# Kernel optimization log

Measured on AMD Instinct MI355X. Metric: run time of the kernel, lower is better.

Reference implementation:

```python
import jax, jax.numpy as jnp
import numpy as np

B, S, E, H, MAXLEN = 2, 2048, 1024, 16, 2048


def _level_indices(seq_len: int, base: int = 2) -> np.ndarray:
    """Vectorized version of get_level_index_weak over the full (target, source) grid.
    indices[t, s] = min(level, 2) for s < t, else 0. Runs in O(log S) passes."""
    tt = np.broadcast_to(np.arange(seq_len)[:, None], (seq_len, seq_len)).astype(np.int64).copy()
    ss = np.broadcast_to(np.arange(seq_len)[None, :], (seq_len, seq_len)).astype(np.int64).copy()
    res = np.zeros((seq_len, seq_len), np.int64)
    done = ~(ss < tt)  # only source < target positions get a level; rest stay 0
    while not done.all():
        l = np.floor(np.log2(np.maximum(tt, 1).astype(np.float64))).astype(np.int64)
        v = (np.int64(1) << l)
        hit = (~done) & (ss < v)
        res[hit] = l[hit] + 1
        done |= hit
        step = ~done
        tt[step] -= v[step]
        ss[step] -= v[step]
    return np.minimum(res, 2).astype(np.int32)


def setup_inputs() -> dict:
    key = jax.random.key(0)
    ks = jax.random.split(key, 10)
    sc = 0.02
    return {
        "x": jax.random.normal(ks[0], (B, S, E), dtype=jnp.float32),
        "attention_mask": jax.random.randint(ks[1], (B, S), 0, 2, dtype=jnp.int32),
        "level_indices": jnp.asarray(_level_indices(S, 2)),
        "Wq": jax.random.normal(ks[2], (E, E), dtype=jnp.float32) * sc,
        "bq": jnp.zeros((E,), jnp.float32),
        "Wk": jax.random.normal(ks[3], (E, E), dtype=jnp.float32) * sc,
        "bk": jnp.zeros((E,), jnp.float32),
        "Wv": jax.random.normal(ks[4], (E, E), dtype=jnp.float32) * sc,
        "bv": jnp.zeros((E,), jnp.float32),
        "hier": jax.random.normal(ks[5], (MAXLEN, H, 3), dtype=jnp.float32),
        "Wo": jax.random.normal(ks[6], (E, E), dtype=jnp.float32) * sc,
        "bo": jnp.zeros((E,), jnp.float32),
    }


def reference(x, attention_mask, level_indices, Wq, bq, Wk, bk, Wv, bv, hier, Wo, bo):
    b, s, e = x.shape
    h = hier.shape[1]
    dh = e // h
    # q/k are computed by the original module but never used; kept for fidelity (zero grads).
    q = x @ Wq.T + bq
    k = x @ Wk.T + bk
    v = (x @ Wv.T + bv).reshape(b, s, h, dh).transpose(0, 2, 1, 3)  # [B,H,S,Dh]
    lev = level_indices[:s, :s]  # [S,S] int, values in {0,1,2}
    # Faithful torch.gather semantics: weights[b,h,i,j] = hier[b, h, lev[i,j]]
    w3 = hier[:b]                      # [B,H,3]
    weights = w3[:, :, lev]            # [B,H,S,S]
    decay = jnp.power(jnp.float32(0.5), lev.astype(x.dtype))  # [S,S]
    weights = weights * decay
    weights = weights / (jnp.sum(weights, axis=-1, keepdims=True) + 1e-8)
    weights = jnp.where(attention_mask[:, None, None, :] == 0, jnp.float32(0.0), weights)
    out = jnp.einsum('bhij,bhjd->bhid', weights, v)  # [B,H,S,Dh]
    out = out.transpose(0, 2, 1, 3).reshape(b, s, e)
    return out @ Wo.T + bo
```

## Files before the change

### kernel.cpp

```cpp
#include <hip/hip_runtime.h>
#include <cstdint>
#include <cstddef>

constexpr int Sn = 2048;
constexpr int En = 1024;
constexpr int Bn = 2;
constexpr int Hn = 16;
constexpr int NCH = 32;
constexpr int CHUNK = 64;
constexpr int Mtot = Bn * Sn;
constexpr int GCH = Mtot / CHUNK;

typedef __bf16 bf16x8 __attribute__((ext_vector_type(8)));
typedef float  f32x4  __attribute__((ext_vector_type(4)));

__device__ __forceinline__ unsigned short f2bf(float f) {
    union { float f; uint32_t u; } v; v.f = f;
    const uint32_t u = v.u;
    return (unsigned short)((u + 0x7fffu + ((u >> 16) & 1u)) >> 16);
}
__device__ __forceinline__ float bf2f_lo(uint32_t u) {
    union { uint32_t u; float f; } v; v.u = u << 16; return v.f;
}
__device__ __forceinline__ float bf2f_hi(uint32_t u) {
    union { uint32_t u; float f; } v; v.u = u & 0xffff0000u; return v.f;
}

constexpr int XN = Bn * Sn * En;
constexpr int WN = En * En;

__global__ __launch_bounds__(256)
void cast3(const float* __restrict__ x, const float* __restrict__ Wv,
           const float* __restrict__ Wo, unsigned short* __restrict__ xb,
           unsigned short* __restrict__ Wvb, unsigned short* __restrict__ Wob)
{
    const int i = (blockIdx.x * 256 + threadIdx.x) * 4;
    const float* src; unsigned short* dst; int off;
    if (i < XN)           { src = x;  dst = xb;  off = i; }
    else if (i < XN + WN) { src = Wv; dst = Wvb; off = i - XN; }
    else                  { src = Wo; dst = Wob; off = i - XN - WN; }
    const float4 v = *(const float4*)(src + off);
    ushort4 o;
    o.x = f2bf(v.x); o.y = f2bf(v.y); o.z = f2bf(v.z); o.w = f2bf(v.w);
    *(ushort4*)(dst + off) = o;
}

#define LOAD6(k0, r0, r1, r2, r3, r4, r5)            \
    r0 = *(const uint4*)(gA0 + (k0));                \
    r1 = *(const uint4*)(gA0 + (k0) + 32);           \
    r2 = *(const uint4*)(gA1 + (k0));                \
    r3 = *(const uint4*)(gA1 + (k0) + 32);           \
    r4 = *(const uint4*)(gB0 + (k0));                \
    r5 = *(const uint4*)(gB0 + (k0) + 32);

#define STORE6(r0, r1, r2, r3, r4, r5)               \
    *lA00 = r0; *lA01 = r1;                          \
    *lA10 = r2; *lA11 = r3;                          \
    *lB00 = r4; *lB01 = r5;

#define COMPUTE()                                                                              \
    {                                                                                          \
        bf16x8 af[4][2], bfr[2][2];                                                            \
        _Pragma("unroll")                                                                      \
        for (int i = 0; i < 4; ++i)                                                            \
            _Pragma("unroll")                                                                  \
            for (int kh = 0; kh < 2; ++kh)                                                     \
                af[i][kh] = *(const bf16x8*)&As[((wr * 4 + i) * 2 + kh) * 512 + lane * 8];      \
        _Pragma("unroll")                                                                      \
        for (int j = 0; j < 2; ++j)                                                            \
            _Pragma("unroll")                                                                  \
            for (int kh = 0; kh < 2; ++kh)                                                     \
                bfr[j][kh] = *(const bf16x8*)&Bs[((wc * 2 + j) * 2 + kh) * 512 + lane * 8];     \
        _Pragma("unroll")                                                                      \
        for (int kh = 0; kh < 2; ++kh)                                                         \
            _Pragma("unroll")                                                                  \
            for (int i = 0; i < 4; ++i)                                                        \
                _Pragma("unroll")                                                              \
                for (int j = 0; j < 2; ++j)                                                    \
                    acc[i][j] = __builtin_amdgcn_mfma_f32_16x16x32_bf16(af[i][kh], bfr[j][kh], \
                                                                        acc[i][j], 0, 0, 0);   \
    }

template<bool APPLY_MASK, bool OUT_BF16, bool FUSE_CSUM>
__global__ __launch_bounds__(256)
void gemm_pipe(const unsigned short* __restrict__ A, const unsigned short* __restrict__ Bw,
               const float* __restrict__ bias, const int* __restrict__ mask,
               void* __restrict__ Cv, float* __restrict__ csum, int M, int N, int K)
{
    __shared__ __align__(16) unsigned short As[128 * 64];
    __shared__ __align__(16) unsigned short Bs[64 * 64];

    const int tid  = threadIdx.x;
    const int lane = tid & 63;
    const int wv   = tid >> 6;
    const int wr   = wv >> 1;
    const int wc   = wv & 1;
    const int bm   = blockIdx.y * 128;
    const int bn   = blockIdx.x * 64;
    const int m16  = lane & 15;
    const int kq   = lane >> 4;

    f32x4 acc[4][2] = {};

    const int rg0 = 2 * wv, rg1 = 2 * wv + 1;
    const unsigned short* gA0 = A  + (size_t)(bm + 16 * rg0 + m16) * K + kq * 8;
    const unsigned short* gA1 = A  + (size_t)(bm + 16 * rg1 + m16) * K + kq * 8;
    const unsigned short* gB0 = Bw + (size_t)(bn + 16 * wv  + m16) * K + kq * 8;
    uint4* lA00 = (uint4*)&As[(rg0 * 2 + 0) * 512 + lane * 8];
    uint4* lA01 = (uint4*)&As[(rg0 * 2 + 1) * 512 + lane * 8];
    uint4* lA10 = (uint4*)&As[(rg1 * 2 + 0) * 512 + lane * 8];
    uint4* lA11 = (uint4*)&As[(rg1 * 2 + 1) * 512 + lane * 8];
    uint4* lB00 = (uint4*)&Bs[(wv  * 2 + 0) * 512 + lane * 8];
    uint4* lB01 = (uint4*)&Bs[(wv  * 2 + 1) * 512 + lane * 8];

    uint4 p0, p1, p2, p3, p4, p5;
    uint4 q0, q1, q2, q3, q4, q5;

    LOAD6(0, p0, p1, p2, p3, p4, p5);
#pragma unroll 1
    for (int it = 0; it < 8; ++it) {
        const int kbase = it * 128;
        __syncthreads();
        STORE6(p0, p1, p2, p3, p4, p5);
        __syncthreads();
        LOAD6(kbase + 64, q0, q1, q2, q3, q4, q5);
        COMPUTE();

        __syncthreads();
        STORE6(q0, q1, q2, q3, q4, q5);
        __syncthreads();
        if (it < 7) { LOAD6(kbase + 128, p0, p1, p2, p3, p4, p5); }
        COMPUTE();
    }

    float colsum[2] = {0.0f, 0.0f};
#pragma unroll
    for (int i = 0; i < 4; ++i) {
        const int r0 = bm + wr * 64 + i * 16 + kq * 4;
#pragma unroll
        for (int j = 0; j < 2; ++j) {
            const int c0 = bn + wc * 32 + j * 16 + m16;
            const float bcol = bias[c0];
#pragma unroll
            for (int r = 0; r < 4; ++r) {
                const int row = r0 + r;
                float val = acc[i][j][r] + bcol;
                if (APPLY_MASK) val = (mask[row] == 0) ? 0.0f : val;
                if (FUSE_CSUM) colsum[j] += val;
                if (OUT_BF16)
                    ((unsigned short*)Cv)[(size_t)row * N + c0] = f2bf(val);
                else
                    ((float*)Cv)[(size_t)row * N + c0] = val;
            }
        }
    }

    if (FUSE_CSUM) {
        const int gc = 2 * blockIdx.y + wr;
#pragma unroll
        for (int j = 0; j < 2; ++j) {
            float s = colsum[j];
            s += __shfl_xor(s, 16, 64);
            s += __shfl_xor(s, 32, 64);
            if (kq == 0)
                csum[(size_t)gc * En + bn + wc * 32 + j * 16 + m16] = s;
        }
    }
}

__global__ __launch_bounds__(256)
void combine(const unsigned short* __restrict__ vm, const float* __restrict__ csum,
             const float* __restrict__ hier, unsigned short* __restrict__ opre)
{
    const int ep = blockIdx.x * 256 + threadIdx.x;
    const int e = ep * 2;
    const int c = blockIdx.y;
    const int b = blockIdx.z;
    const int h = e >> 6;

    const float w0 = hier[((size_t)b * Hn + h) * 3 + 0];
    const float w1 = hier[((size_t)b * Hn + h) * 3 + 1] * 0.5f;
    const float w2 = hier[((size_t)b * Hn + h) * 3 + 2] * 0.25f;

    float run0 = 0.0f, run1 = 0.0f, T0 = 0.0f, T1 = 0.0f;
    const int g0 = b * NCH;
    for (int c2 = 0; c2 < NCH; ++c2) {
        const size_t off = (size_t)(g0 + c2) * En + e;
        const float v0 = csum[off], v1 = csum[off + 1];
        if (c2 < c) { run0 += v0; run1 += v1; }
        T0 += v0; T1 += v1;
    }

    float prev0 = 0.0f, prev1 = 0.0f;
    const size_t base = ((size_t)b * Sn + c * CHUNK) * En + e;

    for (int t = 0; t < CHUNK; ++t) {
        const int i = c * CHUNK + t;
        const uint32_t u = *(const uint32_t*)(vm + base + (size_t)t * En);
        const float cur0 = bf2f_lo(u), cur1 = bf2f_hi(u);
        float num0, num1, Z;
        if (i & 1) {
            num0 = w2 * (run0 - prev0) + w1 * prev0 + w0 * (T0 - run0);
            num1 = w2 * (run1 - prev1) + w1 * prev1 + w0 * (T1 - run1);
            Z = (float)(i - 1) * w2 + w1 + (float)(Sn - i) * w0 + 1e-8f;
        } else {
            num0 = w2 * run0 + w0 * (T0 - run0);
            num1 = w2 * run1 + w0 * (T1 - run1);
            Z = (float)i * w2 + (float)(Sn - i) * w0 + 1e-8f;
        }
        const float rz = 1.0f / Z;
        const uint32_t o = (uint32_t)f2bf(num0 * rz) | ((uint32_t)f2bf(num1 * rz) << 16);
        *(uint32_t*)(opre + base + (size_t)t * En) = o;
        run0 += cur0; run1 += cur1;
        prev0 = cur0; prev1 = cur1;
    }
}

extern "C" void kernel_launch(void* const* d_in, const int* in_sizes, int n_in,
                              void* d_out, int out_size, void* d_ws, size_t ws_size,
                              hipStream_t stream)
{
    const float* x    = (const float*)d_in[0];
    const int*   mask = (const int*)d_in[1];
    const float* Wv   = (const float*)d_in[7];
    const float* bv   = (const float*)d_in[8];
    const float* hier = (const float*)d_in[9];
    const float* Wo   = (const float*)d_in[10];
    const float* bo   = (const float*)d_in[11];
    float* out = (float*)d_out;

    const int M = Mtot, N = En, K = En;

    char* ws = (char*)d_ws;
    unsigned short* xb    = (unsigned short*)ws;  ws += (size_t)M * K * 2;
    unsigned short* Wvb   = (unsigned short*)ws;  ws += (size_t)N * K * 2;
    unsigned short* Wob   = (unsigned short*)ws;  ws += (size_t)N * K * 2;
    unsigned short* vmb   = (unsigned short*)ws;  ws += (size_t)M * N * 2;
    float*          csum  = (float*)ws;           ws += (size_t)GCH * En * 4;
    unsigned short* opreb = (unsigned short*)ws;  ws += (size_t)M * N * 2;

    dim3 threads(256);

    cast3<<<dim3((XN + 2 * WN) / 1024), threads, 0, stream>>>(x, Wv, Wo, xb, Wvb, Wob);

    dim3 gemm_grid(N / 64, M / 128);

    gemm_pipe<true, true, true><<<gemm_grid, threads, 0, stream>>>(xb, Wvb, bv, mask, vmb, csum, M, N, K);
    combine<<<dim3(En / 512, NCH, Bn), threads, 0, stream>>>(vmb, csum, hier, opreb);
    gemm_pipe<false, false, false><<<gemm_grid, threads, 0, stream>>>(opreb, Wob, bo, nullptr, out, nullptr, M, N, K);
}
```

Baseline: 170.3 us.

## Remap GEMM blocks per XCD and use one element per thread in combine

The GEMM block index is remapped so that blocks dispatched round-robin to the same XCD cover a contiguous band of row tiles, which is meant to improve L2 reuse of A and B tiles within each XCD. The combine kernel now handles one element per thread instead of two and launches twice as many blocks, trading vectorized 32-bit accesses for more parallelism. The grid is hardcoded to 16x32, which ties the swizzle to the fixed problem size. Division replaces the reciprocal multiply.

```diff
diff --git a/kernel.cpp b/kernel.cpp
--- a/kernel.cpp
+++ b/kernel.cpp
@@ -19,11 +19,8 @@
     const uint32_t u = v.u;
     return (unsigned short)((u + 0x7fffu + ((u >> 16) & 1u)) >> 16);
 }
-__device__ __forceinline__ float bf2f_lo(uint32_t u) {
-    union { uint32_t u; float f; } v; v.u = u << 16; return v.f;
-}
-__device__ __forceinline__ float bf2f_hi(uint32_t u) {
-    union { uint32_t u; float f; } v; v.u = u & 0xffff0000u; return v.f;
+__device__ __forceinline__ float bf2f(unsigned short s) {
+    union { uint32_t u; float f; } v; v.u = (uint32_t)s << 16; return v.f;
 }
 
 constexpr int XN = Bn * Sn * En;
@@ -95,8 +92,13 @@
     const int wv   = tid >> 6;
     const int wr   = wv >> 1;
     const int wc   = wv & 1;
-    const int bm   = blockIdx.y * 128;
-    const int bn   = blockIdx.x * 64;
+    const int id   = blockIdx.y * 16 + blockIdx.x;
+    const int xcd  = id & 7;
+    const int slot = id >> 3;
+    const int by   = xcd * 4 + (slot >> 4);
+    const int bx   = slot & 15;
+    const int bm   = by * 128;
+    const int bn   = bx * 64;
     const int m16  = lane & 15;
     const int kq   = lane >> 4;
 
@@ -156,7 +158,7 @@
     }
 
     if (FUSE_CSUM) {
-        const int gc = 2 * blockIdx.y + wr;
+        const int gc = 2 * by + wr;
 #pragma unroll
         for (int j = 0; j < 2; ++j) {
             float s = colsum[j];
@@ -172,8 +174,7 @@
 void combine(const unsigned short* __restrict__ vm, const float* __restrict__ csum,
              const float* __restrict__ hier, unsigned short* __restrict__ opre)
 {
-    const int ep = blockIdx.x * 256 + threadIdx.x;
-    const int e = ep * 2;
+    const int e = blockIdx.x * 256 + threadIdx.x;
     const int c = blockIdx.y;
     const int b = blockIdx.z;
     const int h = e >> 6;
@@ -182,37 +183,31 @@
     const float w1 = hier[((size_t)b * Hn + h) * 3 + 1] * 0.5f;
     const float w2 = hier[((size_t)b * Hn + h) * 3 + 2] * 0.25f;
 
-    float run0 = 0.0f, run1 = 0.0f, T0 = 0.0f, T1 = 0.0f;
+    float run = 0.0f, T = 0.0f;
     const int g0 = b * NCH;
     for (int c2 = 0; c2 < NCH; ++c2) {
-        const size_t off = (size_t)(g0 + c2) * En + e;
-        const float v0 = csum[off], v1 = csum[off + 1];
-        if (c2 < c) { run0 += v0; run1 += v1; }
-        T0 += v0; T1 += v1;
-    }
-
-    float prev0 = 0.0f, prev1 = 0.0f;
+        const float v = csum[(size_t)(g0 + c2) * En + e];
+        if (c2 < c) run += v;
+        T += v;
+    }
+
+    float prev = 0.0f;
     const size_t base = ((size_t)b * Sn + c * CHUNK) * En + e;
 
     for (int t = 0; t < CHUNK; ++t) {
         const int i = c * CHUNK + t;
-        const uint32_t u = *(const uint32_t*)(vm + base + (size_t)t * En);
-        const float cur0 = bf2f_lo(u), cur1 = bf2f_hi(u);
-        float num0, num1, Z;
+        const float cur = bf2f(vm[base + (size_t)t * En]);
+        float num, Z;
         if (i & 1) {
-            num0 = w2 * (run0 - prev0) + w1 * prev0 + w0 * (T0 - run0);
-            num1 = w2 * (run1 - prev1) + w1 * prev1 + w0 * (T1 - run1);
+            num = w2 * (run - prev) + w1 * prev + w0 * (T - run);
             Z = (float)(i - 1) * w2 + w1 + (float)(Sn - i) * w0 + 1e-8f;
         } else {
-            num0 = w2 * run0 + w0 * (T0 - run0);
-            num1 = w2 * run1 + w0 * (T1 - run1);
+            num = w2 * run + w0 * (T - run);
             Z = (float)i * w2 + (float)(Sn - i) * w0 + 1e-8f;
         }
-        const float rz = 1.0f / Z;
-        const uint32_t o = (uint32_t)f2bf(num0 * rz) | ((uint32_t)f2bf(num1 * rz) << 16);
-        *(uint32_t*)(opre + base + (size_t)t * En) = o;
-        run0 += cur0; run1 += cur1;
-        prev0 = cur0; prev1 = cur1;
+        opre[base + (size_t)t * En] = f2bf(num / Z);
+        run += cur;
+        prev = cur;
     }
 }
 
@@ -243,9 +238,9 @@
 
     cast3<<<dim3((XN + 2 * WN) / 1024), threads, 0, stream>>>(x, Wv, Wo, xb, Wvb, Wob);
 
-    dim3 gemm_grid(N / 64, M / 128);
+    dim3 gemm_grid(16, 32);
 
     gemm_pipe<true, true, true><<<gemm_grid, threads, 0, stream>>>(xb, Wvb, bv, mask, vmb, csum, M, N, K);
-    combine<<<dim3(En / 512, NCH, Bn), threads, 0, stream>>>(vmb, csum, hier, opreb);
+    combine<<<dim3(En / 256, NCH, Bn), threads, 0, stream>>>(vmb, csum, hier, opreb);
     gemm_pipe<false, false, false><<<gemm_grid, threads, 0, stream>>>(opreb, Wob, bo, nullptr, out, nullptr, M, N, K);
 }
```

After: 169.1 us. Within noise of the previous version (-0.7%).
